# Kernel tuning notes

Hardware: AMD Instinct MI355X
Metric: run time of the kernel (lower is better)

## Reference

```python
import jax, jax.numpy as jnp
import numpy as np

THINK_STEPS = 15
MAX_ANSWER_SZ = 30


def setup_inputs() -> dict:
    key = jax.random.key(0)
    ks = jax.random.split(key, 6)
    V, H, B, SQ = 95, 2048, 256, 162
    s = 1.0 / np.sqrt(H)
    x = jax.random.randint(ks[0], (B, SQ), 0, V, dtype=jnp.int64)
    W_ih = jax.random.uniform(ks[1], (4 * H, V), jnp.float32, -s, s)
    W_hh = jax.random.uniform(ks[2], (4 * H, H), jnp.float32, -s, s)
    b_ih = jax.random.uniform(ks[3], (4 * H,), jnp.float32, -s, s)
    b_hh = jax.random.uniform(ks[4], (4 * H,), jnp.float32, -s, s)
    W_proj = jax.random.uniform(ks[5], (V, H), jnp.float32, -s, s)
    return {"x": x, "W_ih": W_ih, "W_hh": W_hh, "b_ih": b_ih, "b_hh": b_hh, "W_proj": W_proj}


def reference(x, W_ih, W_hh, b_ih, b_hh, W_proj):
    V = W_ih.shape[1]
    H = W_hh.shape[1]
    B = x.shape[0]
    bias = b_ih + b_hh

    def cell(h, c, inp):
        # PyTorch gate order: i, f, g, o
        g = inp @ W_ih.T + h @ W_hh.T + bias  # (B, 4H)
        i, f, gg, o = jnp.split(g, 4, axis=-1)
        c_new = jax.nn.sigmoid(f) * c + jax.nn.sigmoid(i) * jnp.tanh(gg)
        h_new = jax.nn.sigmoid(o) * jnp.tanh(c_new)
        return h_new, c_new

    # Phase 1: consume one-hot question, seq-major (SQ, B, V)
    xs = jax.nn.one_hot(x.T, V, dtype=jnp.float32)
    h0 = jnp.zeros((B, H), jnp.float32)
    c0 = jnp.zeros((B, H), jnp.float32)

    def q_step(carry, xt):
        h, c = carry
        h, c = cell(h, c, xt)
        return (h, c), None

    (h, c), _ = jax.lax.scan(q_step, (h0, c0), xs)
    out_q = h  # `outputs` after question loop; NOT updated during thinking

    # Phase 2: 15 zero-input "thinking" steps (only state updated)
    zero_in = jnp.zeros((B, V), jnp.float32)

    def t_step(carry, _):
        h, c = carry
        h, c = cell(h, c, zero_in)
        return (h, c), None

    (h, c), _ = jax.lax.scan(t_step, (h, c), None, length=THINK_STEPS)

    def a_step(carry, _):
        out, h, c = carry
        logits = out @ W_proj.T  # (B, V)
        h_new, c_new = cell(h, c, logits)
        return (h_new, h_new, c_new), logits

    _, output_seq = jax.lax.scan(a_step, (out_q, h, c), None, length=MAX_ANSWER_SZ - 1)
    return output_seq.reshape(-1, V)  # ((A-1)*B, V)
```

## Files before the change

### kernel.cpp

```cpp
#include <hip/hip_runtime.h>


#define Hdim 2048
#define G4H  8192
#define Bsz  256
#define Vsz  95
#define SQL  162
#define TSTEPS 15
#define ASTEPS 29

typedef signed char i8;
typedef __attribute__((ext_vector_type(4))) int i32x4;

#define S_RANGE 0.0220970869121f
#define SWI (127.0f / S_RANGE)
#define SG  (S_RANGE / (127.0f * 127.0f))

__device__ __forceinline__ float sigm(float x) { return 1.0f / (1.0f + expf(-x)); }

__device__ __forceinline__ void quant2(float xl, i8& q1, i8& q2) {
  float a = rintf(xl);
  q1 = (i8)(int)a;
  q2 = (i8)(int)rintf((xl - a) * 128.0f);
}

#define LGKM_BAR                                            \
  asm volatile("s_waitcnt lgkmcnt(0)" ::: "memory");        \
  __builtin_amdgcn_s_barrier();

__global__ void k_split2(const float* __restrict__ w, i8* __restrict__ w1,
                         i8* __restrict__ w2) {
  for (long i = blockIdx.x * blockDim.x + threadIdx.x; i < (long)G4H * Hdim;
       i += (long)gridDim.x * blockDim.x) {
    int n = (int)(i >> 11), k = (int)(i & 2047);
    long r = (long)((n & 3) * Hdim + (n >> 2));
    float xl = w[r * Hdim + k] * SWI;
    i8 a, b;
    quant2(xl, a, b);
    w1[i] = a;
    w2[i] = b;
  }
}

__global__ void k_prep(const float* __restrict__ W_ih, const float* __restrict__ b_ih,
                       const float* __restrict__ b_hh, float* __restrict__ wihT2,
                       float* __restrict__ bias2, float* __restrict__ hf,
                       i8* __restrict__ h1, i8* __restrict__ h2) {
  int i = blockIdx.x * 256 + threadIdx.x;
  if (i < Vsz * G4H) {
    int v = i / G4H, n = i % G4H;
    int r = (n & 3) * Hdim + (n >> 2);
    wihT2[i] = W_ih[(long)r * Vsz + v];
  }
  if (i < G4H) {
    int r = (i & 3) * Hdim + (i >> 2);
    bias2[i] = b_ih[r] + b_hh[r];
  }
  if (i < Bsz * Hdim) {
    hf[i] = 0.f;
    h1[i] = 0;
    h2[i] = 0;
  }
}

__global__ __launch_bounds__(256) void k_step(
    const i8* __restrict__ a1p, const i8* __restrict__ a2p,
    const i8* __restrict__ b1p, const i8* __restrict__ b2p,
    const float* __restrict__ bias2, const float* __restrict__ wihT2,
    const float* __restrict__ lgp, const int* __restrict__ x, int tstep,
    int xstride, int mode, float* __restrict__ c, float* __restrict__ hf,
    i8* __restrict__ o1, i8* __restrict__ o2) {
  __shared__ __align__(16) i8 SM[32768];

  const int tid = threadIdx.x;
  const int wave = tid >> 6, lane = tid & 63;

  const int lin = blockIdx.x;
  const int lin2 = (lin & 7) * 64 + (lin >> 3);
  const int row0 = (lin2 & 3) * 64;
  const int col0 = (lin2 >> 2) * 64;

  const int wr = wave >> 1, wc = wave & 1;
  const int lr = lane & 15, lc = lane >> 4;

  const i8* gsrc[4];
  i8* wdst[4];
  {
    const int rr = lane >> 2;
    const int koff = ((lane & 3) ^ (rr & 3) ^ ((rr >> 2) & 3)) * 16;
#pragma unroll
    for (int j = 0; j < 4; ++j) {
      int cc = wave * 4 + j;
      const i8* base;
      long rg;
      if (cc < 4)       { base = a1p; rg = row0 + cc * 16; }
      else if (cc < 8)  { base = a2p; rg = row0 + (cc - 4) * 16; }
      else if (cc < 12) { base = b1p; rg = col0 + (cc - 8) * 16; }
      else              { base = b2p; rg = col0 + (cc - 12) * 16; }
      gsrc[j] = base + (rg + rr) * (long)Hdim + koff;
      wdst[j] = SM + cc * 1024 + lane * 16;
    }
  }

  const int sl = (lc ^ (lr & 3) ^ ((lr >> 2) & 3)) * 16;
  int aoff[2], boff[2];
#pragma unroll
  for (int mf = 0; mf < 2; ++mf) aoff[mf] = (wr * 32 + mf * 16 + lr) * 64 + sl;
#pragma unroll
  for (int nf = 0; nf < 2; ++nf) boff[nf] = 8192 + (wc * 32 + nf * 16 + lr) * 64 + sl;

  i32x4 acc1[2][2] = {};
  i32x4 acc2[2][2] = {};
  const char* smb = (const char*)SM;
  i32x4 qA[4], qB[4], qC[4];

#define LOADQ(q, s)                                                   \
  { _Pragma("unroll") for (int j = 0; j < 4; ++j)                     \
        q[j] = *(const i32x4*)(gsrc[j] + (long)(s) * 64); }
#define WRITEQ(q, s)                                                  \
  { _Pragma("unroll") for (int j = 0; j < 4; ++j)                     \
        *(i32x4*)(wdst[j] + (((s) & 1) * 16384)) = q[j]; }

#define COMPUTE(kb)                                                             \
  {                                                                             \
    const char* sb = smb + ((kb) & 1) * 16384;                                  \
    i32x4 A10 = *(const i32x4*)(sb + aoff[0]);                                  \
    i32x4 A11 = *(const i32x4*)(sb + aoff[1]);                                  \
    i32x4 A20 = *(const i32x4*)(sb + 4096 + aoff[0]);                           \
    i32x4 A21 = *(const i32x4*)(sb + 4096 + aoff[1]);                           \
    i32x4 B10 = *(const i32x4*)(sb + boff[0]);                                  \
    i32x4 B11 = *(const i32x4*)(sb + boff[1]);                                  \
    i32x4 B20 = *(const i32x4*)(sb + 4096 + boff[0]);                           \
    i32x4 B21 = *(const i32x4*)(sb + 4096 + boff[1]);                           \
    __builtin_amdgcn_s_setprio(1);                                              \
    acc1[0][0] = __builtin_amdgcn_mfma_i32_16x16x64_i8(A10, B10, acc1[0][0], 0, 0, 0); \
    acc1[0][1] = __builtin_amdgcn_mfma_i32_16x16x64_i8(A10, B11, acc1[0][1], 0, 0, 0); \
    acc1[1][0] = __builtin_amdgcn_mfma_i32_16x16x64_i8(A11, B10, acc1[1][0], 0, 0, 0); \
    acc1[1][1] = __builtin_amdgcn_mfma_i32_16x16x64_i8(A11, B11, acc1[1][1], 0, 0, 0); \
    acc2[0][0] = __builtin_amdgcn_mfma_i32_16x16x64_i8(A10, B20, acc2[0][0], 0, 0, 0); \
    acc2[0][1] = __builtin_amdgcn_mfma_i32_16x16x64_i8(A10, B21, acc2[0][1], 0, 0, 0); \
    acc2[1][0] = __builtin_amdgcn_mfma_i32_16x16x64_i8(A11, B20, acc2[1][0], 0, 0, 0); \
    acc2[1][1] = __builtin_amdgcn_mfma_i32_16x16x64_i8(A11, B21, acc2[1][1], 0, 0, 0); \
    acc2[0][0] = __builtin_amdgcn_mfma_i32_16x16x64_i8(A20, B10, acc2[0][0], 0, 0, 0); \
    acc2[0][1] = __builtin_amdgcn_mfma_i32_16x16x64_i8(A20, B11, acc2[0][1], 0, 0, 0); \
    acc2[1][0] = __builtin_amdgcn_mfma_i32_16x16x64_i8(A21, B10, acc2[1][0], 0, 0, 0); \
    acc2[1][1] = __builtin_amdgcn_mfma_i32_16x16x64_i8(A21, B11, acc2[1][1], 0, 0, 0); \
    __builtin_amdgcn_s_setprio(0);                                              \
  }

  LOADQ(qA, 0); LOADQ(qB, 1); LOADQ(qC, 2);
  WRITEQ(qA, 0);
  LGKM_BAR;

  for (int t5 = 0; t5 < 5; ++t5) {
    const int kb0 = t5 * 6;
    if (kb0 + 3 <= 31) LOADQ(qA, kb0 + 3);
    WRITEQ(qB, kb0 + 1); COMPUTE(kb0); LGKM_BAR;
    if (kb0 + 4 <= 31) LOADQ(qB, kb0 + 4);
    WRITEQ(qC, kb0 + 2); COMPUTE(kb0 + 1); LGKM_BAR;
    if (kb0 + 5 <= 31) LOADQ(qC, kb0 + 5);
    WRITEQ(qA, kb0 + 3); COMPUTE(kb0 + 2); LGKM_BAR;
    if (kb0 + 6 <= 31) LOADQ(qA, kb0 + 6);
    WRITEQ(qB, kb0 + 4); COMPUTE(kb0 + 3); LGKM_BAR;
    if (kb0 + 7 <= 31) LOADQ(qB, kb0 + 7);
    WRITEQ(qC, kb0 + 5); COMPUTE(kb0 + 4); LGKM_BAR;
    if (kb0 + 8 <= 31) LOADQ(qC, kb0 + 8);
    WRITEQ(qA, kb0 + 6); COMPUTE(kb0 + 5); LGKM_BAR;
  }
  WRITEQ(qB, 31); COMPUTE(30); LGKM_BAR;
  COMPUTE(31);

  __syncthreads();
  float* gt = (float*)SM;
#pragma unroll
  for (int mf = 0; mf < 2; ++mf)
#pragma unroll
    for (int nf = 0; nf < 2; ++nf) {
      int col = wc * 32 + nf * 16 + lr;
#pragma unroll
      for (int i = 0; i < 4; ++i) {
        int row = wr * 32 + mf * 16 + lc * 4 + i;
        gt[row * 68 + col] =
            ((float)acc1[mf][nf][i] + (float)acc2[mf][nf][i] * 0.0078125f) * SG;
      }
    }
  __syncthreads();

  const int h16 = tid & 15;
  const int bl16 = tid >> 4;
  const int hh_g = (col0 >> 2) + h16;
  const float bi = bias2[col0 + 4 * h16 + 0];
  const float bf_ = bias2[col0 + 4 * h16 + 1];
  const float bg_ = bias2[col0 + 4 * h16 + 2];
  const float bo = bias2[col0 + 4 * h16 + 3];

  float ai[4] = {0, 0, 0, 0}, af[4] = {0, 0, 0, 0};
  float ag[4] = {0, 0, 0, 0}, ao[4] = {0, 0, 0, 0};
  if (mode == 2) {
    const float* wv0 = wihT2 + col0 + 4 * h16;
    for (int v = 0; v < Vsz; ++v) {
      const float* w4 = wv0 + (long)v * G4H;
      float w0 = w4[0], w1 = w4[1], w2 = w4[2], w3 = w4[3];
#pragma unroll
      for (int pr = 0; pr < 4; ++pr) {
        float l = lgp[(row0 + pr * 16 + bl16) * Vsz + v];
        ai[pr] += l * w0; af[pr] += l * w1; ag[pr] += l * w2; ao[pr] += l * w3;
      }
    }
  }

#pragma unroll
  for (int pr = 0; pr < 4; ++pr) {
    int brow = pr * 16 + bl16;
    int bg = row0 + brow;
    const float* gr = &gt[brow * 68 + 4 * h16];
    float xi = gr[0] + bi + ai[pr], xf = gr[1] + bf_ + af[pr];
    float xg = gr[2] + bg_ + ag[pr], xo = gr[3] + bo + ao[pr];
    if (mode == 1) {
      int tok = x[(bg * SQL + tstep) * xstride];
      const float* wv = wihT2 + (long)tok * G4H + col0 + 4 * h16;
      xi += wv[0]; xf += wv[1]; xg += wv[2]; xo += wv[3];
    }
    long ci = (long)bg * Hdim + hh_g;
    float cn = sigm(xf) * c[ci] + sigm(xi) * tanhf(xg);
    float hn = sigm(xo) * tanhf(cn);
    c[ci] = cn;
    hf[ci] = hn;
    i8 q1, q2;
    quant2(hn * 127.0f, q1, q2);
    o1[ci] = q1;
    o2[ci] = q2;
  }
#undef LOADQ
#undef WRITEQ
#undef COMPUTE
}

__global__ __launch_bounds__(256) void k_logits(const float* __restrict__ src,
                                                const float* __restrict__ Wp,
                                                float* __restrict__ lg,
                                                float* __restrict__ outp) {
  const int b0 = blockIdx.x * 4, tid = threadIdx.x;
  const int wv = tid >> 6, ln = tid & 63;

  float4 hreg[4][8];
#pragma unroll
  for (int r = 0; r < 4; ++r) {
    const float4* srcv = (const float4*)(src + (long)(b0 + r) * Hdim);
#pragma unroll
    for (int i = 0; i < 8; ++i) hreg[r][i] = srcv[ln + 64 * i];
  }

  for (int v = wv; v < Vsz; v += 4) {
    const float4* wrow = (const float4*)(Wp + (long)v * Hdim);
    float s0 = 0.f, s1 = 0.f, s2 = 0.f, s3 = 0.f;
#pragma unroll
    for (int i = 0; i < 8; ++i) {
      float4 w = wrow[ln + 64 * i];
      s0 += w.x * hreg[0][i].x + w.y * hreg[0][i].y + w.z * hreg[0][i].z + w.w * hreg[0][i].w;
      s1 += w.x * hreg[1][i].x + w.y * hreg[1][i].y + w.z * hreg[1][i].z + w.w * hreg[1][i].w;
      s2 += w.x * hreg[2][i].x + w.y * hreg[2][i].y + w.z * hreg[2][i].z + w.w * hreg[2][i].w;
      s3 += w.x * hreg[3][i].x + w.y * hreg[3][i].y + w.z * hreg[3][i].z + w.w * hreg[3][i].w;
    }
#pragma unroll
    for (int off = 32; off; off >>= 1) {
      s0 += __shfl_down(s0, off);
      s1 += __shfl_down(s1, off);
      s2 += __shfl_down(s2, off);
      s3 += __shfl_down(s3, off);
    }
    if (ln == 0) {
      lg[(b0 + 0) * Vsz + v] = s0;
      lg[(b0 + 1) * Vsz + v] = s1;
      lg[(b0 + 2) * Vsz + v] = s2;
      lg[(b0 + 3) * Vsz + v] = s3;
      outp[(b0 + 0) * Vsz + v] = s0;
      outp[(b0 + 1) * Vsz + v] = s1;
      outp[(b0 + 2) * Vsz + v] = s2;
      outp[(b0 + 3) * Vsz + v] = s3;
    }
  }
}

extern "C" void kernel_launch(void* const* d_in, const int* in_sizes, int n_in,
                              void* d_out, int out_size, void* d_ws, size_t ws_size,
                              hipStream_t stream) {
  const int* x = (const int*)d_in[0];
  const float* W_ih = (const float*)d_in[1];
  const float* W_hh = (const float*)d_in[2];
  const float* b_ih = (const float*)d_in[3];
  const float* b_hh = (const float*)d_in[4];
  const float* W_proj = (const float*)d_in[5];
  float* out = (float*)d_out;

  int xstride = (in_sizes[0] > Bsz * SQL) ? 2 : 1;

  i8* w1 = (i8*)d_ws;
  i8* w2 = w1 + (long)G4H * Hdim;
  float* wihT2 = (float*)(w2 + (long)G4H * Hdim);
  float* bias2 = wihT2 + (long)Vsz * G4H;
  float* hf = bias2 + G4H;
  float* c = hf + (long)Bsz * Hdim;
  float* outq = c + (long)Bsz * Hdim;
  float* lg = outq + (long)Bsz * Hdim;
  i8* h1A = (i8*)(lg + Bsz * Vsz);
  i8* h2A = h1A + (long)Bsz * Hdim;
  i8* h1B = h2A + (long)Bsz * Hdim;
  i8* h2B = h1B + (long)Bsz * Hdim;

  k_split2<<<4096, 256, 0, stream>>>(W_hh, w1, w2);
  k_prep<<<3040, 256, 0, stream>>>(W_ih, b_ih, b_hh, wihT2, bias2, hf, h1A, h2A);

  hipMemsetAsync(c, 0, (long)Bsz * Hdim * sizeof(float), stream);

  i8* i1[2] = {h1A, h1B};
  i8* i2[2] = {h2A, h2B};
  int pp = 0;

  for (int t = 0; t < SQL; ++t) {
    k_step<<<512, 256, 0, stream>>>(i1[pp], i2[pp], w1, w2, bias2, wihT2,
                                    nullptr, x, t, xstride, 1, c, hf,
                                    i1[pp ^ 1], i2[pp ^ 1]);
    pp ^= 1;
  }
  hipMemcpyAsync(outq, hf, (long)Bsz * Hdim * sizeof(float),
                 hipMemcpyDeviceToDevice, stream);

  for (int t = 0; t < TSTEPS; ++t) {
    k_step<<<512, 256, 0, stream>>>(i1[pp], i2[pp], w1, w2, bias2, wihT2,
                                    nullptr, nullptr, 0, 1, 0, c, hf,
                                    i1[pp ^ 1], i2[pp ^ 1]);
    pp ^= 1;
  }

  for (int s = 0; s < ASTEPS; ++s) {
    const float* src = (s == 0) ? outq : hf;
    k_logits<<<64, 256, 0, stream>>>(src, W_proj, lg, out + (long)s * Bsz * Vsz);
    k_step<<<512, 256, 0, stream>>>(i1[pp], i2[pp], w1, w2, bias2, wihT2,
                                    lg, nullptr, 0, 1, 2, c, hf,
                                    i1[pp ^ 1], i2[pp ^ 1]);
    pp ^= 1;
  }
}
```

Measured before the change: 5.973 ms.

## Enlarge step-kernel tile to 128 rows with 512 threads and 128-wide K slices

Each block of the recurrent step kernel now computes a 128x64 output tile with 512 threads instead of a 64x64 tile with 256 threads. The K loop moves 128 bytes per stage in two halves, over 16 stages instead of 32, and shared memory grows to 96KB. The aim is to read the W_hh tiles from global memory half as often and to cut the number of barrier-separated pipeline stages. In exchange the grid halves to 256 blocks, which may leave some CUs idle, and the large shared memory footprint limits occupancy.

```diff
diff --git a/kernel.cpp b/kernel.cpp
--- a/kernel.cpp
+++ b/kernel.cpp
@@ -63,41 +63,42 @@
   }
 }
 
-__global__ __launch_bounds__(256) void k_step(
+__global__ __launch_bounds__(512) void k_step(
     const i8* __restrict__ a1p, const i8* __restrict__ a2p,
     const i8* __restrict__ b1p, const i8* __restrict__ b2p,
     const float* __restrict__ bias2, const float* __restrict__ wihT2,
     const float* __restrict__ lgp, const int* __restrict__ x, int tstep,
     int xstride, int mode, float* __restrict__ c, float* __restrict__ hf,
     i8* __restrict__ o1, i8* __restrict__ o2) {
-  __shared__ __align__(16) i8 SM[32768];
+  __shared__ __align__(16) i8 SM[98304];
 
   const int tid = threadIdx.x;
   const int wave = tid >> 6, lane = tid & 63;
 
   const int lin = blockIdx.x;
-  const int lin2 = (lin & 7) * 64 + (lin >> 3);
-  const int row0 = (lin2 & 3) * 64;
-  const int col0 = (lin2 >> 2) * 64;
+  const int lin2 = (lin & 7) * 32 + (lin >> 3);
+  const int row0 = (lin2 & 1) * 128;
+  const int col0 = (lin2 >> 1) * 64;
 
   const int wr = wave >> 1, wc = wave & 1;
   const int lr = lane & 15, lc = lane >> 4;
 
-  const i8* gsrc[4];
-  i8* wdst[4];
+  const i8* gsrc[6];
+  i8* wdst[6];
   {
     const int rr = lane >> 2;
     const int koff = ((lane & 3) ^ (rr & 3) ^ ((rr >> 2) & 3)) * 16;
 #pragma unroll
-    for (int j = 0; j < 4; ++j) {
-      int cc = wave * 4 + j;
+    for (int j = 0; j < 6; ++j) {
+      int cc = wave * 6 + j;
+      int half = cc / 24, c24 = cc % 24;
       const i8* base;
       long rg;
-      if (cc < 4)       { base = a1p; rg = row0 + cc * 16; }
-      else if (cc < 8)  { base = a2p; rg = row0 + (cc - 4) * 16; }
-      else if (cc < 12) { base = b1p; rg = col0 + (cc - 8) * 16; }
-      else              { base = b2p; rg = col0 + (cc - 12) * 16; }
-      gsrc[j] = base + (rg + rr) * (long)Hdim + koff;
+      if (c24 < 8)       { base = a1p; rg = row0 + c24 * 16; }
+      else if (c24 < 16) { base = a2p; rg = row0 + (c24 - 8) * 16; }
+      else if (c24 < 20) { base = b1p; rg = col0 + (c24 - 16) * 16; }
+      else               { base = b2p; rg = col0 + (c24 - 20) * 16; }
+      gsrc[j] = base + (rg + rr) * (long)Hdim + half * 64 + koff;
       wdst[j] = SM + cc * 1024 + lane * 16;
     }
   }
@@ -107,27 +108,26 @@
 #pragma unroll
   for (int mf = 0; mf < 2; ++mf) aoff[mf] = (wr * 32 + mf * 16 + lr) * 64 + sl;
 #pragma unroll
-  for (int nf = 0; nf < 2; ++nf) boff[nf] = 8192 + (wc * 32 + nf * 16 + lr) * 64 + sl;
+  for (int nf = 0; nf < 2; ++nf) boff[nf] = 16384 + (wc * 32 + nf * 16 + lr) * 64 + sl;
 
   i32x4 acc1[2][2] = {};
   i32x4 acc2[2][2] = {};
   const char* smb = (const char*)SM;
-  i32x4 qA[4], qB[4], qC[4];
+  i32x4 qA[6], qB[6], qC[6];
 
 #define LOADQ(q, s)                                                   \
-  { _Pragma("unroll") for (int j = 0; j < 4; ++j)                     \
-        q[j] = *(const i32x4*)(gsrc[j] + (long)(s) * 64); }
+  { _Pragma("unroll") for (int j = 0; j < 6; ++j)                     \
+        q[j] = *(const i32x4*)(gsrc[j] + (long)(s) * 128); }
 #define WRITEQ(q, s)                                                  \
-  { _Pragma("unroll") for (int j = 0; j < 4; ++j)                     \
-        *(i32x4*)(wdst[j] + (((s) & 1) * 16384)) = q[j]; }
-
-#define COMPUTE(kb)                                                             \
+  { _Pragma("unroll") for (int j = 0; j < 6; ++j)                     \
+        *(i32x4*)(wdst[j] + (((s) & 1) * 49152)) = q[j]; }
+
+#define HALF(sb)                                                                \
   {                                                                             \
-    const char* sb = smb + ((kb) & 1) * 16384;                                  \
     i32x4 A10 = *(const i32x4*)(sb + aoff[0]);                                  \
     i32x4 A11 = *(const i32x4*)(sb + aoff[1]);                                  \
-    i32x4 A20 = *(const i32x4*)(sb + 4096 + aoff[0]);                           \
-    i32x4 A21 = *(const i32x4*)(sb + 4096 + aoff[1]);                           \
+    i32x4 A20 = *(const i32x4*)(sb + 8192 + aoff[0]);                           \
+    i32x4 A21 = *(const i32x4*)(sb + 8192 + aoff[1]);                           \
     i32x4 B10 = *(const i32x4*)(sb + boff[0]);                                  \
     i32x4 B11 = *(const i32x4*)(sb + boff[1]);                                  \
     i32x4 B20 = *(const i32x4*)(sb + 4096 + boff[0]);                           \
@@ -148,27 +148,27 @@
     __builtin_amdgcn_s_setprio(0);                                              \
   }
 
+#define COMPUTE(kb)                                         \
+  {                                                         \
+    const char* sb0 = smb + ((kb) & 1) * 49152;             \
+    HALF(sb0);                                              \
+    HALF((sb0 + 24576));                                    \
+  }
+
   LOADQ(qA, 0); LOADQ(qB, 1); LOADQ(qC, 2);
   WRITEQ(qA, 0);
   LGKM_BAR;
 
-  for (int t5 = 0; t5 < 5; ++t5) {
-    const int kb0 = t5 * 6;
-    if (kb0 + 3 <= 31) LOADQ(qA, kb0 + 3);
-    WRITEQ(qB, kb0 + 1); COMPUTE(kb0); LGKM_BAR;
-    if (kb0 + 4 <= 31) LOADQ(qB, kb0 + 4);
-    WRITEQ(qC, kb0 + 2); COMPUTE(kb0 + 1); LGKM_BAR;
-    if (kb0 + 5 <= 31) LOADQ(qC, kb0 + 5);
-    WRITEQ(qA, kb0 + 3); COMPUTE(kb0 + 2); LGKM_BAR;
-    if (kb0 + 6 <= 31) LOADQ(qA, kb0 + 6);
-    WRITEQ(qB, kb0 + 4); COMPUTE(kb0 + 3); LGKM_BAR;
-    if (kb0 + 7 <= 31) LOADQ(qB, kb0 + 7);
-    WRITEQ(qC, kb0 + 5); COMPUTE(kb0 + 4); LGKM_BAR;
-    if (kb0 + 8 <= 31) LOADQ(qC, kb0 + 8);
-    WRITEQ(qA, kb0 + 6); COMPUTE(kb0 + 5); LGKM_BAR;
-  }
-  WRITEQ(qB, 31); COMPUTE(30); LGKM_BAR;
-  COMPUTE(31);
+  for (int t3 = 0; t3 < 4; ++t3) {
+    const int kb0 = t3 * 3;
+    LOADQ(qA, kb0 + 3); WRITEQ(qB, kb0 + 1); COMPUTE(kb0); LGKM_BAR;
+    LOADQ(qB, kb0 + 4); WRITEQ(qC, kb0 + 2); COMPUTE(kb0 + 1); LGKM_BAR;
+    LOADQ(qC, kb0 + 5); WRITEQ(qA, kb0 + 3); COMPUTE(kb0 + 2); LGKM_BAR;
+  }
+  LOADQ(qA, 15); WRITEQ(qB, 13); COMPUTE(12); LGKM_BAR;
+  WRITEQ(qC, 14); COMPUTE(13); LGKM_BAR;
+  WRITEQ(qA, 15); COMPUTE(14); LGKM_BAR;
+  COMPUTE(15);
 
   __syncthreads();
   float* gt = (float*)SM;
@@ -187,7 +187,7 @@
   __syncthreads();
 
   const int h16 = tid & 15;
-  const int bl16 = tid >> 4;
+  const int bl32 = tid >> 4;
   const int hh_g = (col0 >> 2) + h16;
   const float bi = bias2[col0 + 4 * h16 + 0];
   const float bf_ = bias2[col0 + 4 * h16 + 1];
@@ -203,7 +203,7 @@
       float w0 = w4[0], w1 = w4[1], w2 = w4[2], w3 = w4[3];
 #pragma unroll
       for (int pr = 0; pr < 4; ++pr) {
-        float l = lgp[(row0 + pr * 16 + bl16) * Vsz + v];
+        float l = lgp[(row0 + pr * 32 + bl32) * Vsz + v];
         ai[pr] += l * w0; af[pr] += l * w1; ag[pr] += l * w2; ao[pr] += l * w3;
       }
     }
@@ -211,7 +211,7 @@
 
 #pragma unroll
   for (int pr = 0; pr < 4; ++pr) {
-    int brow = pr * 16 + bl16;
+    int brow = pr * 32 + bl32;
     int bg = row0 + brow;
     const float* gr = &gt[brow * 68 + 4 * h16];
     float xi = gr[0] + bi + ai[pr], xf = gr[1] + bf_ + af[pr];
@@ -233,6 +233,7 @@
   }
 #undef LOADQ
 #undef WRITEQ
+#undef HALF
 #undef COMPUTE
 }
 
@@ -318,7 +319,7 @@
   int pp = 0;
 
   for (int t = 0; t < SQL; ++t) {
-    k_step<<<512, 256, 0, stream>>>(i1[pp], i2[pp], w1, w2, bias2, wihT2,
+    k_step<<<256, 512, 0, stream>>>(i1[pp], i2[pp], w1, w2, bias2, wihT2,
                                     nullptr, x, t, xstride, 1, c, hf,
                                     i1[pp ^ 1], i2[pp ^ 1]);
     pp ^= 1;
@@ -327,7 +328,7 @@
                  hipMemcpyDeviceToDevice, stream);
 
   for (int t = 0; t < TSTEPS; ++t) {
-    k_step<<<512, 256, 0, stream>>>(i1[pp], i2[pp], w1, w2, bias2, wihT2,
+    k_step<<<256, 512, 0, stream>>>(i1[pp], i2[pp], w1, w2, bias2, wihT2,
                                     nullptr, nullptr, 0, 1, 0, c, hf,
                                     i1[pp ^ 1], i2[pp ^ 1]);
     pp ^= 1;
@@ -336,7 +337,7 @@
   for (int s = 0; s < ASTEPS; ++s) {
     const float* src = (s == 0) ? outq : hf;
     k_logits<<<64, 256, 0, stream>>>(src, W_proj, lg, out + (long)s * Bsz * Vsz);
-    k_step<<<512, 256, 0, stream>>>(i1[pp], i2[pp], w1, w2, bias2, wihT2,
+    k_step<<<256, 512, 0, stream>>>(i1[pp], i2[pp], w1, w2, bias2, wihT2,
                                     lg, nullptr, 0, 1, 2, c, hf,
                                     i1[pp ^ 1], i2[pp ^ 1]);
     pp ^= 1;
```

Measured after the change: 5.924 ms. About the same (-0.8%).
